# Optimization experiments

Hardware: AMD Instinct MI355X
Metric: run time of the kernel (lower is better)

The kernel has to match this reference:

```python
import jax, jax.numpy as jnp
import numpy as np

NEG_SLOPE = 0.2

def setup_inputs() -> dict:
    key = jax.random.key(0)
    k1, k2, k3, k4 = jax.random.split(key, 4)
    B, n, d_in, d_out = 8, 2048, 128, 128
    x = jax.random.normal(k1, (B, n, d_in), dtype=jnp.float32)
    adj = jax.random.uniform(k2, (B, n, n), dtype=jnp.float32)
    # glorot init for W: std = sqrt(2/(fan_in+fan_out))
    W = jax.random.normal(k3, (d_in, d_out), dtype=jnp.float32) * np.sqrt(2.0 / (d_in + d_out))
    a = jax.random.normal(k4, (2 * d_out,), dtype=jnp.float32) * np.sqrt(2.0 / (2 * d_out + 1))
    return {"x": x, "adj": adj, "W": W, "a": a}

def reference(x, adj, W, a):
    d_out = W.shape[1]
    h = jnp.einsum('bni,io->bno', x, W)               # [B,n,d_out]
    x_weighted = jnp.einsum('bnm,bmo->bno', adj, h)   # adj @ Wx
    # additive attention: a @ concat(h_i, h_j) == h_i@a_src + h_j@a_dst
    a_src, a_dst = a[:d_out], a[d_out:]
    s_i = h @ a_src                                   # [B,n]
    s_j = h @ a_dst                                   # [B,n]
    e = jax.nn.leaky_relu(s_i[:, :, None] + s_j[:, None, :], NEG_SLOPE)  # [B,n,n]
    alpha = jax.nn.softmax(e, axis=2)
    out = jnp.einsum('bnm,bmo->bno', alpha, h) + x_weighted
    return jax.nn.leaky_relu(out, NEG_SLOPE)
```

## Files before the change

kernel.cpp:

```cpp
#include <hip/hip_runtime.h>
#include <hip/hip_bf16.h>

#define NEG 0.2f
#define LOG2E 1.4426950408889634f

typedef __attribute__((ext_vector_type(8))) short bf16x8;
typedef __attribute__((ext_vector_type(4))) float f32x4;
typedef __attribute__((ext_vector_type(4))) int int4v;

__device__ __forceinline__ float lrelu(float t){ return fmaxf(t, NEG * t); }
__device__ __forceinline__ float fast_exp2(float x){
  float r; asm("v_exp_f32 %0, %1" : "=v"(r) : "v"(x)); return r;
}
__device__ __forceinline__ unsigned short f2bf(float f){
  union { float f; unsigned int u; } v; v.f = f;
  unsigned int r = v.u + 0x7FFFu + ((v.u >> 16) & 1u);
  return (unsigned short)(r >> 16);
}

__global__ __launch_bounds__(256) void k1_fused(const float* __restrict__ x,
                                                const float* __restrict__ W,
                                                const float* __restrict__ a,
                                                unsigned short* __restrict__ ht,
                                                float* __restrict__ ssrcL,
                                                float* __restrict__ sdstL){
  __shared__ __align__(16) float Wl[128*128];
  __shared__ __align__(16) float xl[32*136];
  __shared__ __align__(16) unsigned short tl[128*34];
  const int t = threadIdx.x;
  const int bx = blockIdx.x;
  const int b  = bx >> 6;
  const int jt = bx & 63;
  const long rowbase = (long)bx * 32;
  {
    const f32x4* W4 = (const f32x4*)W;
    f32x4* Wl4 = (f32x4*)Wl;
#pragma unroll
    for (int i = 0; i < 16; ++i) Wl4[t + 256*i] = W4[t + 256*i];
    const int r = t >> 3, seg = t & 7;
    const f32x4* xs = (const f32x4*)(x + (rowbase + r)*128 + seg*16);
    f32x4* xd = (f32x4*)(xl + r*136 + seg*16);
#pragma unroll
    for (int i = 0; i < 4; ++i) xd[i] = xs[i];
  }
  __syncthreads();
  const int r = t >> 3, c = t & 7;
  f32x4 zro = {0.f, 0.f, 0.f, 0.f};
  f32x4 a0 = zro, a1 = zro, a2 = zro, a3 = zro;
  const float* xr = xl + r*136;
#pragma unroll 4
  for (int k = 0; k < 128; ++k){
    const float xv = xr[k];
    const f32x4* wk = (const f32x4*)(Wl + k*128 + c*16);
    a0 += xv * wk[0]; a1 += xv * wk[1]; a2 += xv * wk[2]; a3 += xv * wk[3];
  }
  {
    const f32x4* as4 = (const f32x4*)(a + c*16);
    const f32x4* ad4 = (const f32x4*)(a + 128 + c*16);
    f32x4 s0 = a0*as4[0] + a1*as4[1] + a2*as4[2] + a3*as4[3];
    f32x4 d0 = a0*ad4[0] + a1*ad4[1] + a2*ad4[2] + a3*ad4[3];
    float ps = s0[0]+s0[1]+s0[2]+s0[3];
    float pd = d0[0]+d0[1]+d0[2]+d0[3];
    ps += __shfl_down(ps, 4); pd += __shfl_down(pd, 4);
    ps += __shfl_down(ps, 2); pd += __shfl_down(pd, 2);
    ps += __shfl_down(ps, 1); pd += __shfl_down(pd, 1);
    if (c == 0){
      ssrcL[rowbase + r] = ps * LOG2E;
      sdstL[rowbase + r] = pd * LOG2E;
    }
  }
  {
    float hv[16];
    *(f32x4*)&hv[0] = a0; *(f32x4*)&hv[4] = a1; *(f32x4*)&hv[8] = a2; *(f32x4*)&hv[12] = a3;
#pragma unroll
    for (int e = 0; e < 16; ++e) tl[(c*16 + e)*34 + r] = f2bf(hv[e]);
  }
  __syncthreads();
  {
    const int o = t >> 1, jseg = (t & 1) * 16;
    const unsigned int* src = (const unsigned int*)(tl + o*34 + jseg);
    unsigned int p[8];
#pragma unroll
    for (int i = 0; i < 8; ++i) p[i] = src[i];
    unsigned short* dst = ht + (long)b*262144 + (long)o*2048 + jt*32 + jseg;
    ((int4v*)dst)[0] = *(int4v*)&p[0];
    ((int4v*)dst)[1] = *(int4v*)&p[4];
  }
}

__global__ __launch_bounds__(256) void k2_ml(const float* __restrict__ ssrcL,
                                             const float* __restrict__ sdstL,
                                             float* __restrict__ carr){
  const int lane = threadIdx.x & 63;
  const long row = (long)blockIdx.x * 4 + (threadIdx.x >> 6);
  const int b = (int)(row >> 11);
  const float siL = ssrcL[row];
  const float* sd = sdstL + (long)b*2048;
  float mx = -3.4e38f;
#pragma unroll
  for (int k = 0; k < 8; ++k){
    f32x4 v = *(const f32x4*)(sd + lane*4 + k*256);
    mx = fmaxf(mx, fmaxf(fmaxf(v[0], v[1]), fmaxf(v[2], v[3])));
  }
#pragma unroll
  for (int off = 1; off <= 32; off <<= 1) mx = fmaxf(mx, __shfl_xor(mx, off));
  const float mL = lrelu(siL + mx);
  float sum = 0.f;
#pragma unroll
  for (int k = 0; k < 8; ++k){
    f32x4 v = *(const f32x4*)(sd + lane*4 + k*256);
#pragma unroll
    for (int e = 0; e < 4; ++e) sum += fast_exp2(lrelu(siL + v[e]) - mL);
  }
#pragma unroll
  for (int off = 1; off <= 32; off <<= 1) sum += __shfl_xor(sum, off);
  if (lane == 0) carr[row] = mL + __log2f(sum);
}

__global__ __launch_bounds__(512) void k3_main(const float* __restrict__ adj,
                                               const unsigned short* __restrict__ ht,
                                               const float* __restrict__ ssrcL,
                                               const float* __restrict__ sdstL,
                                               const float* __restrict__ carr,
                                               float* __restrict__ out){
  __shared__ __align__(16) unsigned short tl[2][2][128*40];
  __shared__ __align__(16) float red[64*128];
  const int t   = threadIdx.x;
  const int bx  = blockIdx.x;
  const int b   = bx >> 5;
  const int i0  = (bx & 31) * 64;
  const int lane = t & 63;
  const int lr  = lane & 15, hi = lane >> 4;
  const int kh  = t >> 8, wr = (t >> 6) & 3;
  const int rowi = i0 + wr*16 + lr;
  const long rowg = (long)b*2048 + rowi;
  const float siL = ssrcL[rowg];
  const float Ci  = carr[rowg];
  const float* adjrow = adj + rowg*2048 + kh*1024 + hi*8;
  const float* sdb    = sdstL + (long)b*2048 + kh*1024 + hi*8;
  const unsigned short* htg = ht + (long)b*262144;
  const int so = t >> 2, sseg = t & 3;
  const unsigned short* sgp = htg + (long)so*2048 + sseg*8;
  const int woff = so*40 + sseg*8;

  f32x4 zro = {0.f, 0.f, 0.f, 0.f};
  f32x4 acc[8];
#pragma unroll
  for (int i = 0; i < 8; ++i) acc[i] = zro;

  int4v t0a = *(const int4v*)(sgp);
  int4v t0b = *(const int4v*)(sgp + 1024);
  *(int4v*)(&tl[0][0][woff]) = t0a;
  *(int4v*)(&tl[0][1][woff]) = t0b;
  int4v sA0 = *(const int4v*)(sgp + 32);
  int4v sA1 = *(const int4v*)(sgp + 1024 + 32);
  int4v sB0 = *(const int4v*)(sgp + 64);
  int4v sB1 = *(const int4v*)(sgp + 1024 + 64);
  f32x4 aA0 = *(const f32x4*)(adjrow);
  f32x4 aA1 = *(const f32x4*)(adjrow + 4);
  f32x4 dA0 = *(const f32x4*)(sdb);
  f32x4 dA1 = *(const f32x4*)(sdb + 4);
  f32x4 aB0 = *(const f32x4*)(adjrow + 32);
  f32x4 aB1 = *(const f32x4*)(adjrow + 36);
  f32x4 dB0 = *(const f32x4*)(sdb + 32);
  f32x4 dB1 = *(const f32x4*)(sdb + 36);
  asm volatile("s_waitcnt lgkmcnt(0)" ::: "memory");
  __builtin_amdgcn_s_barrier();
  __builtin_amdgcn_sched_barrier(0);

#define K3_ITER(KT, S0, S1, A0, A1, D0, D1, BW, BR)  do{                        \
    *(int4v*)(&tl[BW][0][woff]) = S0;   \
    *(int4v*)(&tl[BW][1][woff]) = S1;                                            \
    {  const int jo3 = ((KT)+3 < 32 ? (KT)+3 : 31)*32;      \
       S0 = *(const int4v*)(sgp + jo3);                                          \
       S1 = *(const int4v*)(sgp + 1024 + jo3); }                                 \
    bf16x8 af;                                                                   \
    {  float w[8];                                                               \
       _Pragma("unroll")                                                         \
       for (int e = 0; e < 4; ++e){                                              \
         const float u0 = siL + D0[e];                                           \
         w[e]     = A0[e] + fast_exp2(lrelu(u0) - Ci);                           \
         const float u1 = siL + D1[e];                                           \
         w[4 + e] = A1[e] + fast_exp2(lrelu(u1) - Ci);                           \
       }                                                                         \
       const unsigned int p01 = __builtin_amdgcn_perm(__float_as_uint(w[1]), __float_as_uint(w[0]), 0x07060302u); \
       const unsigned int p23 = __builtin_amdgcn_perm(__float_as_uint(w[3]), __float_as_uint(w[2]), 0x07060302u); \
       const unsigned int p45 = __builtin_amdgcn_perm(__float_as_uint(w[5]), __float_as_uint(w[4]), 0x07060302u); \
       const unsigned int p67 = __builtin_amdgcn_perm(__float_as_uint(w[7]), __float_as_uint(w[6]), 0x07060302u); \
       int4v ai = {(int)p01, (int)p23, (int)p45, (int)p67};                      \
       af = *(bf16x8*)&ai;                                                       \
    }                                                                            \
    {  const int jn = ((KT)+2 < 32 ? (KT)+2 : 31)*32;       \
       A0 = *(const f32x4*)(adjrow + jn);                                        \
       A1 = *(const f32x4*)(adjrow + jn + 4);                                    \
       D0 = *(const f32x4*)(sdb + jn);                                           \
       D1 = *(const f32x4*)(sdb + jn + 4); }                                     \
    _Pragma("unroll")                                                            \
    for (int cg = 0; cg < 8; ++cg){                                              \
      const bf16x8 bfv = *(const bf16x8*)(&tl[BR][kh][(cg*16 + lr)*40 + hi*8]);  \
      acc[cg] = __builtin_amdgcn_mfma_f32_16x16x32_bf16(af, bfv, acc[cg], 0, 0, 0); \
    }                                                                            \
    asm volatile("s_waitcnt lgkmcnt(0)" ::: "memory");                           \
    __builtin_amdgcn_s_barrier();                                                \
    __builtin_amdgcn_sched_barrier(0);                                           \
  }while(0)

  for (int kt = 0; kt < 32; kt += 2){
    K3_ITER(kt,     sA0, sA1, aA0, aA1, dA0, dA1, 1, 0);
    K3_ITER(kt + 1, sB0, sB1, aB0, aB1, dB0, dB1, 0, 1);
  }
#undef K3_ITER

  if (kh == 1){
#pragma unroll
    for (int cg = 0; cg < 8; ++cg)
#pragma unroll
      for (int q = 0; q < 4; ++q)
        red[(wr*16 + hi*4 + q)*128 + cg*16 + lr] = acc[cg][q];
  }
  __syncthreads();
  if (kh == 0){
#pragma unroll
    for (int cg = 0; cg < 8; ++cg){
#pragma unroll
      for (int q = 0; q < 4; ++q){
        const int rl2 = wr*16 + hi*4 + q;
        const float v = acc[cg][q] + red[rl2*128 + cg*16 + lr];
        out[((long)b*2048 + i0 + rl2)*128 + cg*16 + lr] = lrelu(v);
      }
    }
  }
}

extern "C" void kernel_launch(void* const* d_in, const int* in_sizes, int n_in,
                              void* d_out, int out_size, void* d_ws, size_t ws_size,
                              hipStream_t stream){
  const float* x   = (const float*)d_in[0];
  const float* adj = (const float*)d_in[1];
  const float* W   = (const float*)d_in[2];
  const float* a   = (const float*)d_in[3];
  float* out = (float*)d_out;
  char* ws = (char*)d_ws;

  unsigned short* ht    = (unsigned short*)(ws);
  float*          ssrcL = (float*)(ws + 4194304);
  float*          sdstL = (float*)(ws + 4259840);
  float*          carr  = (float*)(ws + 4325376);

  k1_fused<<<512,  256, 0, stream>>>(x, W, a, ht, ssrcL, sdstL);
  k2_ml   <<<4096, 256, 0, stream>>>(ssrcL, sdstL, carr);
  k3_main <<<256,  512, 0, stream>>>(adj, ht, ssrcL, sdstL, carr, out);
}
```

Baseline: 64.61 us.

## Use bf16 MFMA for x@W projection and halve k3 block size

Adds a tiny kernel that transposes W to bf16, then rewrites the projection kernel to compute h with bf16 MFMA instructions and reduce attention scores through shared memory. The main kernel moves to 256-thread blocks covering 32 rows, giving 512 blocks instead of 256. It reuses one shared buffer for both the tiles and the reduction, and raises wave priority around the MFMA loop. The aim is to cut the scalar FP32 matmul cost and improve occupancy and latency hiding in the adj-streaming kernel. The costs are an extra launch, lower precision for x and W, and reloading the ht tiles twice as often across blocks.

Measured after the change: 64.76 us. About the same (+0.2%).

```diff
diff --git a/kernel.cpp b/kernel.cpp
--- a/kernel.cpp
+++ b/kernel.cpp
@@ -18,73 +18,125 @@
   return (unsigned short)(r >> 16);
 }
 
+__global__ __launch_bounds__(256) void k0_wt(const float* __restrict__ W,
+                                             unsigned short* __restrict__ Wt){
+  __shared__ __align__(16) unsigned short wl[128*136];
+  const int t = threadIdx.x;
+  {
+    const int k = t >> 1, oh = (t & 1) * 64;
+#pragma unroll 8
+    for (int e = 0; e < 64; ++e)
+      wl[(oh + e)*136 + k] = f2bf(W[k*128 + oh + e]);
+  }
+  __syncthreads();
+  {
+    const int o = t >> 1, ks = (t & 1) * 64;
+#pragma unroll
+    for (int g = 0; g < 8; ++g){
+      int4v v = *(const int4v*)(wl + o*136 + ks + g*8);
+      *(int4v*)(Wt + o*128 + ks + g*8) = v;
+    }
+  }
+}
+
 __global__ __launch_bounds__(256) void k1_fused(const float* __restrict__ x,
-                                                const float* __restrict__ W,
+                                                const unsigned short* __restrict__ Wt,
                                                 const float* __restrict__ a,
                                                 unsigned short* __restrict__ ht,
                                                 float* __restrict__ ssrcL,
                                                 float* __restrict__ sdstL){
-  __shared__ __align__(16) float Wl[128*128];
-  __shared__ __align__(16) float xl[32*136];
-  __shared__ __align__(16) unsigned short tl[128*34];
+  __shared__ __align__(16) unsigned short wtl[128*136];
+  __shared__ __align__(16) unsigned short xl[32*136];
+  __shared__ __align__(16) unsigned short tlw[128*34];
+  __shared__ float sred[2][4][2][16];
   const int t = threadIdx.x;
   const int bx = blockIdx.x;
   const int b  = bx >> 6;
   const int jt = bx & 63;
   const long rowbase = (long)bx * 32;
   {
-    const f32x4* W4 = (const f32x4*)W;
-    f32x4* Wl4 = (f32x4*)Wl;
-#pragma unroll
-    for (int i = 0; i < 16; ++i) Wl4[t + 256*i] = W4[t + 256*i];
-    const int r = t >> 3, seg = t & 7;
-    const f32x4* xs = (const f32x4*)(x + (rowbase + r)*128 + seg*16);
-    f32x4* xd = (f32x4*)(xl + r*136 + seg*16);
-#pragma unroll
-    for (int i = 0; i < 4; ++i) xd[i] = xs[i];
+    const int o = t >> 1, seg = (t & 1) * 64;
+    const int4v* src = (const int4v*)(Wt + o*128 + seg);
+    int4v* dst = (int4v*)(wtl + o*136 + seg);
+#pragma unroll
+    for (int g = 0; g < 8; ++g) dst[g] = src[g];
+  }
+  {
+    const int i = t >> 3, ks = (t & 7) * 16;
+    const f32x4* src = (const f32x4*)(x + (rowbase + i)*128 + ks);
+    unsigned int q[8];
+#pragma unroll
+    for (int g = 0; g < 4; ++g){
+      f32x4 v = src[g];
+      q[g*2]   = (unsigned)f2bf(v[0]) | ((unsigned)f2bf(v[1]) << 16);
+      q[g*2+1] = (unsigned)f2bf(v[2]) | ((unsigned)f2bf(v[3]) << 16);
+    }
+    int4v* dst = (int4v*)(xl + i*136 + ks);
+    dst[0] = *(int4v*)&q[0];
+    dst[1] = *(int4v*)&q[4];
   }
   __syncthreads();
-  const int r = t >> 3, c = t & 7;
+  const int w = t >> 6, lane = t & 63, lr = lane & 15, hi = lane >> 4;
   f32x4 zro = {0.f, 0.f, 0.f, 0.f};
-  f32x4 a0 = zro, a1 = zro, a2 = zro, a3 = zro;
-  const float* xr = xl + r*136;
-#pragma unroll 4
-  for (int k = 0; k < 128; ++k){
-    const float xv = xr[k];
-    const f32x4* wk = (const f32x4*)(Wl + k*128 + c*16);
-    a0 += xv * wk[0]; a1 += xv * wk[1]; a2 += xv * wk[2]; a3 += xv * wk[3];
-  }
-  {
-    const f32x4* as4 = (const f32x4*)(a + c*16);
-    const f32x4* ad4 = (const f32x4*)(a + 128 + c*16);
-    f32x4 s0 = a0*as4[0] + a1*as4[1] + a2*as4[2] + a3*as4[3];
-    f32x4 d0 = a0*ad4[0] + a1*ad4[1] + a2*ad4[2] + a3*ad4[3];
-    float ps = s0[0]+s0[1]+s0[2]+s0[3];
-    float pd = d0[0]+d0[1]+d0[2]+d0[3];
-    ps += __shfl_down(ps, 4); pd += __shfl_down(pd, 4);
-    ps += __shfl_down(ps, 2); pd += __shfl_down(pd, 2);
-    ps += __shfl_down(ps, 1); pd += __shfl_down(pd, 1);
-    if (c == 0){
-      ssrcL[rowbase + r] = ps * LOG2E;
-      sdstL[rowbase + r] = pd * LOG2E;
-    }
-  }
-  {
-    float hv[16];
-    *(f32x4*)&hv[0] = a0; *(f32x4*)&hv[4] = a1; *(f32x4*)&hv[8] = a2; *(f32x4*)&hv[12] = a3;
-#pragma unroll
-    for (int e = 0; e < 16; ++e) tl[(c*16 + e)*34 + r] = f2bf(hv[e]);
+  f32x4 acc00 = zro, acc01 = zro, acc10 = zro, acc11 = zro;
+#pragma unroll
+  for (int ks = 0; ks < 4; ++ks){
+    const bf16x8 a0 = *(const bf16x8*)(wtl + (w*32      + lr)*136 + ks*32 + hi*8);
+    const bf16x8 a1 = *(const bf16x8*)(wtl + (w*32 + 16 + lr)*136 + ks*32 + hi*8);
+    const bf16x8 b0 = *(const bf16x8*)(xl + (     lr)*136 + ks*32 + hi*8);
+    const bf16x8 b1 = *(const bf16x8*)(xl + (16 + lr)*136 + ks*32 + hi*8);
+    acc00 = __builtin_amdgcn_mfma_f32_16x16x32_bf16(a0, b0, acc00, 0, 0, 0);
+    acc01 = __builtin_amdgcn_mfma_f32_16x16x32_bf16(a0, b1, acc01, 0, 0, 0);
+    acc10 = __builtin_amdgcn_mfma_f32_16x16x32_bf16(a1, b0, acc10, 0, 0, 0);
+    acc11 = __builtin_amdgcn_mfma_f32_16x16x32_bf16(a1, b1, acc11, 0, 0, 0);
+  }
+  {
+    const f32x4 as0 = *(const f32x4*)(a +       w*32      + hi*4);
+    const f32x4 as1 = *(const f32x4*)(a +       w*32 + 16 + hi*4);
+    const f32x4 ad0 = *(const f32x4*)(a + 128 + w*32      + hi*4);
+    const f32x4 ad1 = *(const f32x4*)(a + 128 + w*32 + 16 + hi*4);
+    float ps0, ps1, pd0, pd1;
+    {
+      f32x4 u = acc00*as0 + acc10*as1;  ps0 = u[0]+u[1]+u[2]+u[3];
+      f32x4 v = acc01*as0 + acc11*as1;  ps1 = v[0]+v[1]+v[2]+v[3];
+      f32x4 p = acc00*ad0 + acc10*ad1;  pd0 = p[0]+p[1]+p[2]+p[3];
+      f32x4 r = acc01*ad0 + acc11*ad1;  pd1 = r[0]+r[1]+r[2]+r[3];
+    }
+#pragma unroll
+    for (int off = 16; off <= 32; off <<= 1){
+      ps0 += __shfl_xor(ps0, off); ps1 += __shfl_xor(ps1, off);
+      pd0 += __shfl_xor(pd0, off); pd1 += __shfl_xor(pd1, off);
+    }
+    if (hi == 0){
+      sred[0][w][0][lr] = ps0; sred[0][w][1][lr] = ps1;
+      sred[1][w][0][lr] = pd0; sred[1][w][1][lr] = pd1;
+    }
+  }
+#pragma unroll
+  for (int q = 0; q < 4; ++q){
+    tlw[(w*32      + hi*4 + q)*34      + lr] = f2bf(acc00[q]);
+    tlw[(w*32      + hi*4 + q)*34 + 16 + lr] = f2bf(acc01[q]);
+    tlw[(w*32 + 16 + hi*4 + q)*34      + lr] = f2bf(acc10[q]);
+    tlw[(w*32 + 16 + hi*4 + q)*34 + 16 + lr] = f2bf(acc11[q]);
   }
   __syncthreads();
   {
     const int o = t >> 1, jseg = (t & 1) * 16;
-    const unsigned int* src = (const unsigned int*)(tl + o*34 + jseg);
+    const unsigned int* src = (const unsigned int*)(tlw + o*34 + jseg);
     unsigned int p[8];
 #pragma unroll
-    for (int i = 0; i < 8; ++i) p[i] = src[i];
+    for (int g = 0; g < 8; ++g) p[g] = src[g];
     unsigned short* dst = ht + (long)b*262144 + (long)o*2048 + jt*32 + jseg;
     ((int4v*)dst)[0] = *(int4v*)&p[0];
     ((int4v*)dst)[1] = *(int4v*)&p[4];
+  }
+  if (t < 64){
+    const int sel = t >> 5, jl = t & 31;
+    const int ig = jl >> 4, l2 = jl & 15;
+    const float s = sred[sel][0][ig][l2] + sred[sel][1][ig][l2]
+                  + sred[sel][2][ig][l2] + sred[sel][3][ig][l2];
+    if (sel == 0) ssrcL[rowbase + jl] = s * LOG2E;
+    else          sdstL[rowbase + jl] = s * LOG2E;
   }
 }
 
@@ -117,21 +169,22 @@
   if (lane == 0) carr[row] = mL + __log2f(sum);
 }
 
-__global__ __launch_bounds__(512) void k3_main(const float* __restrict__ adj,
+__global__ __launch_bounds__(256) void k3_main(const float* __restrict__ adj,
                                                const unsigned short* __restrict__ ht,
                                                const float* __restrict__ ssrcL,
                                                const float* __restrict__ sdstL,
                                                const float* __restrict__ carr,
                                                float* __restrict__ out){
-  __shared__ __align__(16) unsigned short tl[2][2][128*40];
-  __shared__ __align__(16) float red[64*128];
+  __shared__ __align__(16) char smem[40960];
+  unsigned short* tl = (unsigned short*)smem;
+  float* red = (float*)smem;
   const int t   = threadIdx.x;
   const int bx  = blockIdx.x;
-  const int b   = bx >> 5;
-  const int i0  = (bx & 31) * 64;
+  const int b   = bx >> 6;
+  const int i0  = (bx & 63) * 32;
   const int lane = t & 63;
   const int lr  = lane & 15, hi = lane >> 4;
-  const int kh  = t >> 8, wr = (t >> 6) & 3;
+  const int kh  = t >> 7, wr = (t >> 6) & 1;
   const int rowi = i0 + wr*16 + lr;
   const long rowg = (long)b*2048 + rowi;
   const float siL = ssrcL[rowg];
@@ -140,22 +193,28 @@
   const float* sdb    = sdstL + (long)b*2048 + kh*1024 + hi*8;
   const unsigned short* htg = ht + (long)b*262144;
   const int so = t >> 2, sseg = t & 3;
-  const unsigned short* sgp = htg + (long)so*2048 + sseg*8;
-  const int woff = so*40 + sseg*8;
+  const unsigned short* sgp0 = htg + (long)so*2048 + sseg*8;
+  const unsigned short* sgp1 = htg + (long)(so + 64)*2048 + sseg*8;
+  const int woff0 = so*40 + sseg*8;
+  const int woff1 = (so + 64)*40 + sseg*8;
 
   f32x4 zro = {0.f, 0.f, 0.f, 0.f};
   f32x4 acc[8];
 #pragma unroll
   for (int i = 0; i < 8; ++i) acc[i] = zro;
 
-  int4v t0a = *(const int4v*)(sgp);
-  int4v t0b = *(const int4v*)(sgp + 1024);
-  *(int4v*)(&tl[0][0][woff]) = t0a;
-  *(int4v*)(&tl[0][1][woff]) = t0b;
-  int4v sA0 = *(const int4v*)(sgp + 32);
-  int4v sA1 = *(const int4v*)(sgp + 1024 + 32);
-  int4v sB0 = *(const int4v*)(sgp + 64);
-  int4v sB1 = *(const int4v*)(sgp + 1024 + 64);
+  *(int4v*)(tl + 0*5120 + woff0) = *(const int4v*)(sgp0);
+  *(int4v*)(tl + 1*5120 + woff0) = *(const int4v*)(sgp0 + 1024);
+  *(int4v*)(tl + 0*5120 + woff1) = *(const int4v*)(sgp1);
+  *(int4v*)(tl + 1*5120 + woff1) = *(const int4v*)(sgp1 + 1024);
+  int4v pA0 = *(const int4v*)(sgp0 + 32);
+  int4v pA1 = *(const int4v*)(sgp0 + 1024 + 32);
+  int4v pA2 = *(const int4v*)(sgp1 + 32);
+  int4v pA3 = *(const int4v*)(sgp1 + 1024 + 32);
+  int4v pB0 = *(const int4v*)(sgp0 + 64);
+  int4v pB1 = *(const int4v*)(sgp0 + 1024 + 64);
+  int4v pB2 = *(const int4v*)(sgp1 + 64);
+  int4v pB3 = *(const int4v*)(sgp1 + 1024 + 64);
   f32x4 aA0 = *(const f32x4*)(adjrow);
   f32x4 aA1 = *(const f32x4*)(adjrow + 4);
   f32x4 dA0 = *(const f32x4*)(sdb);
@@ -168,12 +227,16 @@
   __builtin_amdgcn_s_barrier();
   __builtin_amdgcn_sched_barrier(0);
 
-#define K3_ITER(KT, S0, S1, A0, A1, D0, D1, BW, BR)  do{                        \
-    *(int4v*)(&tl[BW][0][woff]) = S0;   \
-    *(int4v*)(&tl[BW][1][woff]) = S1;                                            \
+#define K3_ITER(KT, P0, P1, P2, P3, A0, A1, D0, D1, BW, BR)  do{                 \
+    *(int4v*)(tl + ((BW)*2+0)*5120 + woff0) = P0;           \
+    *(int4v*)(tl + ((BW)*2+1)*5120 + woff0) = P1;                                \
+    *(int4v*)(tl + ((BW)*2+0)*5120 + woff1) = P2;                                \
+    *(int4v*)(tl + ((BW)*2+1)*5120 + woff1) = P3;                                \
     {  const int jo3 = ((KT)+3 < 32 ? (KT)+3 : 31)*32;      \
-       S0 = *(const int4v*)(sgp + jo3);                                          \
-       S1 = *(const int4v*)(sgp + 1024 + jo3); }                                 \
+       P0 = *(const int4v*)(sgp0 + jo3);                                         \
+       P1 = *(const int4v*)(sgp0 + 1024 + jo3);                                  \
+       P2 = *(const int4v*)(sgp1 + jo3);                                         \
+       P3 = *(const int4v*)(sgp1 + 1024 + jo3); }                                \
     bf16x8 af;                                                                   \
     {  float w[8];                                                               \
        _Pragma("unroll")                                                         \
@@ -195,19 +258,21 @@
        A1 = *(const f32x4*)(adjrow + jn + 4);                                    \
        D0 = *(const f32x4*)(sdb + jn);                                           \
        D1 = *(const f32x4*)(sdb + jn + 4); }                                     \
+    __builtin_amdgcn_s_setprio(1);                                               \
     _Pragma("unroll")                                                            \
     for (int cg = 0; cg < 8; ++cg){                                              \
-      const bf16x8 bfv = *(const bf16x8*)(&tl[BR][kh][(cg*16 + lr)*40 + hi*8]);  \
+      const bf16x8 bfv = *(const bf16x8*)(tl + ((BR)*2+kh)*5120 + (cg*16 + lr)*40 + hi*8); \
       acc[cg] = __builtin_amdgcn_mfma_f32_16x16x32_bf16(af, bfv, acc[cg], 0, 0, 0); \
     }                                                                            \
+    __builtin_amdgcn_s_setprio(0);                                               \
     asm volatile("s_waitcnt lgkmcnt(0)" ::: "memory");                           \
     __builtin_amdgcn_s_barrier();                                                \
     __builtin_amdgcn_sched_barrier(0);                                           \
   }while(0)
 
   for (int kt = 0; kt < 32; kt += 2){
-    K3_ITER(kt,     sA0, sA1, aA0, aA1, dA0, dA1, 1, 0);
-    K3_ITER(kt + 1, sB0, sB1, aB0, aB1, dB0, dB1, 0, 1);
+    K3_ITER(kt,     pA0, pA1, pA2, pA3, aA0, aA1, dA0, dA1, 1, 0);
+    K3_ITER(kt + 1, pB0, pB1, pB2, pB3, aB0, aB1, dB0, dB1, 0, 1);
   }
 #undef K3_ITER
 
@@ -246,8 +311,10 @@
   float*          ssrcL = (float*)(ws + 4194304);
   float*          sdstL = (float*)(ws + 4259840);
   float*          carr  = (float*)(ws + 4325376);
-
-  k1_fused<<<512,  256, 0, stream>>>(x, W, a, ht, ssrcL, sdstL);
+  unsigned short* Wt    = (unsigned short*)(ws + 4390912);
+
+  k0_wt   <<<1,    256, 0, stream>>>(W, Wt);
+  k1_fused<<<512,  256, 0, stream>>>(x, Wt, a, ht, ssrcL, sdstL);
   k2_ml   <<<4096, 256, 0, stream>>>(ssrcL, sdstL, carr);
-  k3_main <<<256,  512, 0, stream>>>(adj, ht, ssrcL, sdstL, carr, out);
-}
+  k3_main <<<512,  256, 0, stream>>>(adj, ht, ssrcL, sdstL, carr, out);
+}
```
